# Kernel optimization log

Measured on AMD Instinct MI355X. Metric: run time of the kernel, lower is better.

## Reference

```python
import jax, jax.numpy as jnp
import numpy as np

D_MODEL = 1024
HEADS = 16
D_K = D_MODEL // HEADS
SCALE = 1.0 / np.sqrt(D_K)


def setup_inputs() -> dict:
    key = jax.random.key(0)
    ks = jax.random.split(key, 12)
    B, S = 4, 2048
    std = 1.0 / np.sqrt(D_MODEL)
    inp = {
        "query": jax.random.normal(ks[0], (B, S, D_MODEL), jnp.float32),
        "key": jax.random.normal(ks[1], (B, S, D_MODEL), jnp.float32),
        "value": jax.random.normal(ks[2], (B, S, D_MODEL), jnp.float32),
        # projection weights stored [in, out] (transpose of torch Linear)
        "Wq": jax.random.normal(ks[3], (D_MODEL, D_MODEL), jnp.float32) * std,
        "bq": jax.random.normal(ks[4], (D_MODEL,), jnp.float32) * std,
        "Wk": jax.random.normal(ks[5], (D_MODEL, D_MODEL), jnp.float32) * std,
        "bk": jax.random.normal(ks[6], (D_MODEL,), jnp.float32) * std,
        "Wv": jax.random.normal(ks[7], (D_MODEL, D_MODEL), jnp.float32) * std,
        "bv": jax.random.normal(ks[8], (D_MODEL,), jnp.float32) * std,
        "Wo": jax.random.normal(ks[9], (D_MODEL, D_MODEL), jnp.float32) * std,
        "bo": jax.random.normal(ks[10], (D_MODEL,), jnp.float32) * std,
    }
    return inp


def _proj(x, W, b):
    # [B,S,D] -> [B,S,H,Dk]
    B, S, _ = x.shape
    return (x @ W + b).reshape(B, S, HEADS, D_K)


def reference(query, key, value, Wq, bq, Wk, bk, Wv, bv, Wo, bo):
    B, S, _ = query.shape
    Q = _proj(query, Wq, bq)
    K = _proj(key, Wk, bk)
    V = _proj(value, Wv, bv)
    scores = jnp.einsum('bihd,bjhd->bijh', Q, K) * SCALE
    # FAITHFUL to original: nn.Softmax(dim=1) normalizes over the QUERY axis i
    attn = jax.nn.softmax(scores, axis=1)
    # dropout is identity at inference
    x = jnp.einsum('bijh,bjhd->bihd', attn, V).reshape(B, S, D_MODEL)
    return x @ Wo + bo
```

## Files before the change

kernel.cpp:

```cpp
#include <hip/hip_runtime.h>


#define B_   4
#define S_   2048
#define D_   1024
#define H_   16
#define DK_  64
#define BH_  64
#define SC2_    0.18033688f

typedef __bf16 bf16x2 __attribute__((ext_vector_type(2)));
typedef __bf16 bf16x4 __attribute__((ext_vector_type(4)));
typedef __bf16 bf16x8 __attribute__((ext_vector_type(8)));
typedef float  f32x4  __attribute__((ext_vector_type(4)));
typedef unsigned int u32;

#define MFMA16(a,b,c) __builtin_amdgcn_mfma_f32_16x16x32_bf16((a),(b),(c),0,0,0)

__device__ __forceinline__ bf16x8 ld8(const __bf16* p){ return *(const bf16x8*)p; }

__device__ __forceinline__ void gll16(const __bf16* g, __bf16* l) {
    __builtin_amdgcn_global_load_lds(
        (const __attribute__((address_space(1))) u32*)g,
        (__attribute__((address_space(3))) u32*)l, 16, 0, 0);
}

#define PIPE_BAR(N) do {                                                      \
    asm volatile("s_waitcnt vmcnt(" #N ") lgkmcnt(0)" ::: "memory");          \
    __builtin_amdgcn_s_barrier();                                             \
    __builtin_amdgcn_sched_barrier(0);                                        \
} while (0)

__global__ __launch_bounds__(256) void wtrans3(
    const float* __restrict__ W0, const float* __restrict__ W1,
    const float* __restrict__ W2, __bf16* __restrict__ Wt)
{
    __shared__ __align__(16) __bf16 Ls[64][80];
    const int t = threadIdx.x;
    const int k0 = blockIdx.x * 64, n0 = blockIdx.y * 64, z = blockIdx.z;
    const float* W = (z == 0) ? W0 : ((z == 1) ? W1 : W2);
    __bf16* out = Wt + (size_t)z * D_ * D_;

#pragma unroll
    for (int p = 0; p < 4; ++p) {
        int id = p*256 + t;
        int k = id >> 4, nq = id & 15;
        f32x4 v = *(const f32x4*)&W[(size_t)(k0 + k)*D_ + n0 + nq*4];
#pragma unroll
        for (int u = 0; u < 4; ++u) Ls[nq*4 + u][k] = (__bf16)v[u];
    }
    __syncthreads();
#pragma unroll
    for (int p = 0; p < 2; ++p) {
        int id = p*256 + t;
        int n = id >> 3, c = id & 7;
        *(bf16x8*)&out[(size_t)(n0 + n)*D_ + k0 + c*8] =
            *(const bf16x8*)&Ls[n][c*8];
    }
}

template<int ABF16, int MODE>
__device__ __forceinline__ void gemm_pipe(
    const void* __restrict__ Ap, const __bf16* __restrict__ Wt,
    const float* __restrict__ bias, void* __restrict__ C,
    float scale, int m0, int n0)
{
    __shared__ __align__(16) __bf16 As[3][128*32];
    __shared__ __align__(16) __bf16 Bs[3][128*32];

    const int t = threadIdx.x, lane = t & 63, w = t >> 6;
    const int wm = w >> 1, wn = w & 1;
    const int fr = lane & 15, fq = lane >> 4;

    const __bf16* Ab = (const __bf16*)Ap;
    const float*  Af = (const float*)Ap;

    f32x4 acc[4][4];
#pragma unroll
    for (int i = 0; i < 4; ++i)
#pragma unroll
        for (int j = 0; j < 4; ++j) acc[i][j] = (f32x4){0.f,0.f,0.f,0.f};

#define PSTAGE_B(kk, bsel)                                                    \
    _Pragma("unroll")                                                         \
    for (int p = 0; p < 2; ++p) {                                             \
        int id = p*256 + t;                                                   \
        int n = id >> 2, l = (id & 3) ^ (n & 3);                              \
        gll16(&Wt[(size_t)(n0 + n)*D_ + (kk) + l*8],                          \
              &Bs[bsel][(size_t)(p*256 + (t & ~63))*8]);                      \
    }

#define PSTAGE_A_BF(kk, bsel)                                                 \
    _Pragma("unroll")                                                         \
    for (int p = 0; p < 2; ++p) {                                             \
        int id = p*256 + t;                                                   \
        int row = id >> 2, l = (id & 3) ^ (row & 3);                          \
        gll16(&Ab[(size_t)(m0 + row)*D_ + (kk) + l*8],                        \
              &As[bsel][(size_t)(p*256 + (t & ~63))*8]);                      \
    }

#define PLOAD_A(kk, xa)                                                       \
    _Pragma("unroll")                                                         \
    for (int p = 0; p < 2; ++p) {                                             \
        int id = p*256 + t;                                                   \
        int row = id >> 2, l = (id & 3) ^ (row & 3);                          \
        const float* ap = &Af[(size_t)(m0 + row)*D_ + (kk) + l*8];            \
        xa[2*p]   = *(const f32x4*)ap;                                        \
        xa[2*p+1] = *(const f32x4*)(ap + 4);                                  \
    }

#define PCVT_WR(xa, bsel)                                                     \
    _Pragma("unroll")                                                         \
    for (int p = 0; p < 2; ++p) {                                             \
        f32x4 x0 = xa[2*p], x1 = xa[2*p+1];                                   \
        bf16x8 v = { (__bf16)x0[0], (__bf16)x0[1], (__bf16)x0[2],             \
                     (__bf16)x0[3], (__bf16)x1[0], (__bf16)x1[1],             \
                     (__bf16)x1[2], (__bf16)x1[3] };                          \
        *(bf16x8*)&As[bsel][(size_t)(p*256 + t)*8] = v;                       \
    }

    f32x4 xa0[4], xa1[4];

    if (ABF16) {
        PSTAGE_A_BF(0, 0)  PSTAGE_B(0, 0)
        PSTAGE_A_BF(32, 1) PSTAGE_B(32, 1)
        PIPE_BAR(4);
    } else {
        PSTAGE_B(0, 0)  PLOAD_A(0, xa0)
        PSTAGE_B(32, 1) PLOAD_A(32, xa1)
        PCVT_WR(xa0, 0)
        PIPE_BAR(6);
    }

#pragma unroll
    for (int tt = 0; tt < 32; ++tt) {
        const int cur = tt % 3, nx1 = (tt + 1) % 3, nx2 = (tt + 2) % 3;

        if (ABF16) {
            if (tt < 30) {
                PSTAGE_A_BF(32*(tt + 2), nx2)
                PSTAGE_B(32*(tt + 2), nx2)
            }
        } else {
            if (tt < 30) {
                PSTAGE_B(32*(tt + 2), nx2)
                if (tt & 1) { PLOAD_A(32*(tt + 2), xa1) }
                else        { PLOAD_A(32*(tt + 2), xa0) }
            }
            if (tt < 31) {
                if (tt & 1) { PCVT_WR(xa0, nx1) }
                else        { PCVT_WR(xa1, nx1) }
            }
        }

        {
            bf16x8 af[4], bfr[4];
#pragma unroll
            for (int mt = 0; mt < 4; ++mt) {
                int row = wm*64 + mt*16 + fr;
                af[mt] = ld8(&As[cur][row*32 + 8*(fq ^ (row & 3))]);
            }
#pragma unroll
            for (int nt = 0; nt < 4; ++nt) {
                int n = wn*64 + nt*16 + fr;
                bfr[nt] = ld8(&Bs[cur][n*32 + 8*(fq ^ (n & 3))]);
            }
#pragma unroll
            for (int mt = 0; mt < 4; ++mt)
#pragma unroll
                for (int nt = 0; nt < 4; ++nt)
                    acc[mt][nt] = MFMA16(af[mt], bfr[nt], acc[mt][nt]);
        }

        if (ABF16) { PIPE_BAR(4); } else { PIPE_BAR(6); }
    }
#undef PSTAGE_B
#undef PSTAGE_A_BF
#undef PLOAD_A
#undef PCVT_WR

#pragma unroll
    for (int mt = 0; mt < 4; ++mt)
#pragma unroll
        for (int nt = 0; nt < 4; ++nt) {
            int colg = n0 + wn*64 + nt*16 + fr;
            float bv = bias[colg];
#pragma unroll
            for (int r = 0; r < 4; ++r) {
                int rowg = m0 + wm*64 + mt*16 + fq*4 + r;
                float o = (acc[mt][nt][r] + bv) * scale;
                if (MODE == 0) {
                    ((float*)C)[(size_t)rowg*D_ + colg] = o;
                } else {
                    int b = rowg >> 11, sp = rowg & (S_-1);
                    int h = colg >> 6, dk = colg & 63;
                    ((__bf16*)C)[(((size_t)(b*H_ + h))*S_ + sp)*DK_ + dk] = (__bf16)o;
                }
            }
        }
}

template<int ABF16, int MODE>
__global__ __launch_bounds__(256) void gemm128(
    const void* __restrict__ Ap, const __bf16* __restrict__ Wt,
    const float* __restrict__ bias, void* __restrict__ C, float scale)
{
    const int gid = blockIdx.x;
    gemm_pipe<ABF16, MODE>(Ap, Wt, bias, C, scale,
                           (gid & 63) * 128, ((gid >> 6) & 7) * 128);
}

__global__ __launch_bounds__(256) void gemm_proj3(
    const float* __restrict__ q, const float* __restrict__ k,
    const float* __restrict__ v, const __bf16* __restrict__ Wt3,
    const float* __restrict__ bq, const float* __restrict__ bk,
    const float* __restrict__ bv,
    __bf16* __restrict__ Qb, __bf16* __restrict__ Kb, __bf16* __restrict__ Vb)
{
    const int gid = blockIdx.x;
    const int z = gid >> 9, inner = gid & 511;
    const float*  A    = (z == 0) ? q  : ((z == 1) ? k  : v);
    const __bf16* Wt   = Wt3 + (size_t)z * D_ * D_;
    const float*  bias = (z == 0) ? bq : ((z == 1) ? bk : bv);
    __bf16*       C    = (z == 0) ? Qb : ((z == 1) ? Kb : Vb);
    const float scale  = (z == 0) ? SC2_ : 1.0f;
    gemm_pipe<0, 1>(A, Wt, bias, C, scale,
                    (inner & 63) * 128, (inner >> 6) * 128);
}

__global__ __launch_bounds__(256) void colsum_rcp(
    const __bf16* __restrict__ Q, const __bf16* __restrict__ K,
    float* __restrict__ Lg)
{
    __shared__ __align__(16) __bf16 Qs[2][64*64];
    const int t = threadIdx.x, lane = t & 63, w = t >> 6;
    const int fr = lane & 15, fq = lane >> 4;
    const int gid = blockIdx.x;
    const int bh = gid & 63;
    const int jw = (gid >> 6)*64 + w*16;
    const __bf16* Qb = Q + (size_t)bh*S_*DK_;
    const __bf16* Kb = K + (size_t)bh*S_*DK_;

    bf16x8 kh0, kh1;
    {
        const __bf16* kr = &Kb[(size_t)(jw + fr)*DK_];
        kh0 = ld8(kr + fq*8);
        kh1 = ld8(kr + 32 + fq*8);
    }

    float accl[4] = {};

#pragma unroll
    for (int p = 0; p < 2; ++p) {
        int c = p*256 + t;
        int i = c >> 3, l = (c & 7) ^ (i & 7);
        gll16(&Qb[(size_t)i*DK_ + l*8], &Qs[0][(size_t)(p*256 + (t & ~63))*8]);
    }
    __syncthreads();

    for (int i0 = 0; i0 < S_; i0 += 64) {
        const int cur = (i0 >> 6) & 1;
        if (i0 + 64 < S_) {
#pragma unroll
            for (int p = 0; p < 2; ++p) {
                int c = p*256 + t;
                int i = c >> 3, l = (c & 7) ^ (i & 7);
                gll16(&Qb[(size_t)(i0 + 64 + i)*DK_ + l*8],
                      &Qs[cur ^ 1][(size_t)(p*256 + (t & ~63))*8]);
            }
        }
#pragma unroll
        for (int it = 0; it < 4; ++it) {
            int i = it*16 + fr;
            bf16x8 q0 = ld8(&Qs[cur][i*64 + 8*(fq ^ (i & 7))]);
            bf16x8 q1 = ld8(&Qs[cur][i*64 + 8*((4 + fq) ^ (i & 7))]);
            f32x4 s = MFMA16(kh0, q0, ((f32x4){0.f,0.f,0.f,0.f}));
            s = MFMA16(kh1, q1, s);
#pragma unroll
            for (int r = 0; r < 4; ++r)
                accl[r] += __builtin_amdgcn_exp2f(s[r]);
        }
        __syncthreads();
    }
#pragma unroll
    for (int r = 0; r < 4; ++r) {
        accl[r] += __shfl_xor(accl[r], 1, 64);
        accl[r] += __shfl_xor(accl[r], 2, 64);
        accl[r] += __shfl_xor(accl[r], 4, 64);
        accl[r] += __shfl_xor(accl[r], 8, 64);
    }
    if (fr == 0) {
#pragma unroll
        for (int r = 0; r < 4; ++r)
            Lg[(size_t)bh*S_ + jw + fq*4 + r] = -__log2f(accl[r]);
    }
}

__global__ __launch_bounds__(512, 4) void attn_pv(
    const __bf16* __restrict__ Q, const __bf16* __restrict__ K,
    const __bf16* __restrict__ V, const float* __restrict__ Lg,
    __bf16* __restrict__ X)
{
    __shared__ __align__(16) __bf16 Ks[2][64*64];
    __shared__ __align__(16) __bf16 Vs[2][64*64];
    __shared__ __align__(16) __bf16 Pl[8][32*64];

    const int t = threadIdx.x, lane = t & 63, w = t >> 6;
    const int fr = lane & 15, fq = lane >> 4;
    const int gid = blockIdx.x;
    const int bh = gid & 63;
    const int iw = (gid >> 6)*256 + w*32;
    const __bf16* Qb = Q + (size_t)bh*S_*DK_;
    const __bf16* Kb = K + (size_t)bh*S_*DK_;
    const __bf16* Vb = V + (size_t)bh*S_*DK_;
    const float*  Rb = Lg + (size_t)bh*S_;

    bf16x8 qf[2][2];
#pragma unroll
    for (int it = 0; it < 2; ++it)
#pragma unroll
        for (int kf = 0; kf < 2; ++kf)
            qf[it][kf] = ld8(&Qb[(size_t)(iw + it*16 + fr)*DK_ + kf*32 + fq*8]);

    const int dq = t & 15, jp = t >> 4;
    const int krow = t >> 3;
    const int kchk = (t & 7) ^ (krow & 7);

    f32x4 acc[2][4];
#pragma unroll
    for (int it = 0; it < 2; ++it)
#pragma unroll
        for (int dt = 0; dt < 4; ++dt) acc[it][dt] = (f32x4){0.f,0.f,0.f,0.f};

    gll16(&Kb[(size_t)krow*DK_ + kchk*8], &Ks[0][(t & ~63)*8]);
    __syncthreads();

    for (int jg = 0; jg < S_; jg += 64) {
        const int cur = (jg >> 6) & 1;

        bf16x4 v0 = *(const bf16x4*)&Vb[(size_t)(jg + 2*jp    )*DK_ + dq*4];
        bf16x4 v1 = *(const bf16x4*)&Vb[(size_t)(jg + 2*jp + 1)*DK_ + dq*4];
        f32x4 lg[4];
#pragma unroll
        for (int jt = 0; jt < 4; ++jt)
            lg[jt] = *(const f32x4*)&Rb[jg + jt*16 + fq*4];
        if (jg + 64 < S_)
            gll16(&Kb[(size_t)(jg + 64 + krow)*DK_ + kchk*8],
                  &Ks[cur ^ 1][(t & ~63)*8]);

#pragma unroll
        for (int jt = 0; jt < 4; ++jt) {
            const __bf16* kb = &Ks[cur][(jt*16 + fr)*64];
            bf16x8 af0 = ld8(kb + ((fq    ) ^ (fr & 7))*8);
            bf16x8 af1 = ld8(kb + ((fq + 4) ^ (fr & 7))*8);
#pragma unroll
            for (int it = 0; it < 2; ++it) {
                f32x4 s = MFMA16(af0, qf[it][0], lg[jt]);
                s = MFMA16(af1, qf[it][1], s);
                bf16x4 pv;
#pragma unroll
                for (int r = 0; r < 4; ++r)
                    pv[r] = (__bf16)__builtin_amdgcn_exp2f(s[r]);
                int il = it*16 + fr;
                *(bf16x4*)&Pl[w][il*64 + (((jt*4 + fq) ^ (2*(fr & 7))))*4] = pv;
            }
        }

#pragma unroll
        for (int u = 0; u < 4; ++u) {
            int d = dq*4 + u;
            int f = (d ^ dq) & 7;
            *(bf16x2*)&Vs[cur][d*64 + (((jp >> 2) ^ f))*8 + (jp & 3)*2] =
                (bf16x2){ v0[u], v1[u] };
        }
        __syncthreads();

        __builtin_amdgcn_s_setprio(1);
#pragma unroll
        for (int kh = 0; kh < 2; ++kh) {
            bf16x8 pa0 = ld8(&Pl[w][(     fr)*64 + (((fq + 4*kh) ^ (fr & 7)))*8]);
            bf16x8 pa1 = ld8(&Pl[w][(16 + fr)*64 + (((fq + 4*kh) ^ (fr & 7)))*8]);
#pragma unroll
            for (int dt = 0; dt < 4; ++dt) {
                int d = dt*16 + fr;
                int f = (d ^ (d >> 2)) & 7;
                bf16x8 vb = ld8(&Vs[cur][d*64 + (((kh*4 + fq) ^ f))*8]);
                acc[0][dt] = MFMA16(pa0, vb, acc[0][dt]);
                acc[1][dt] = MFMA16(pa1, vb, acc[1][dt]);
            }
        }
        __builtin_amdgcn_s_setprio(0);
    }

    const int b = bh >> 4, h = bh & 15;
#pragma unroll
    for (int it = 0; it < 2; ++it)
#pragma unroll
        for (int dt = 0; dt < 4; ++dt)
#pragma unroll
            for (int r = 0; r < 4; ++r) {
                int i = iw + it*16 + fq*4 + r;
                X[((size_t)b*S_ + i)*D_ + h*DK_ + dt*16 + fr] =
                    (__bf16)acc[it][dt][r];
            }
}

extern "C" void kernel_launch(void* const* d_in, const int* in_sizes, int n_in,
                              void* d_out, int out_size, void* d_ws, size_t ws_size,
                              hipStream_t stream)
{
    const float* query = (const float*)d_in[0];
    const float* key   = (const float*)d_in[1];
    const float* value = (const float*)d_in[2];
    const float* Wq = (const float*)d_in[3];  const float* bq = (const float*)d_in[4];
    const float* Wk = (const float*)d_in[5];  const float* bk = (const float*)d_in[6];
    const float* Wv = (const float*)d_in[7];  const float* bv = (const float*)d_in[8];
    const float* Wo = (const float*)d_in[9];  const float* bo = (const float*)d_in[10];

    char* ws = (char*)d_ws;
    char* dob = (char*)d_out;
    const size_t MiB = 1024 * 1024;
    __bf16* Qb = (__bf16*)(ws);
    __bf16* Kb = (__bf16*)(ws + 16 * MiB);
    __bf16* Vb = (__bf16*)(ws + 32 * MiB);
    __bf16* Xb = (__bf16*)(ws + 48 * MiB);
    float*  Lgb = (float*)d_out;
    __bf16* Wt3 = (__bf16*)(dob + 1 * MiB);
    __bf16* WtO = (__bf16*)(ws);

    wtrans3<<<dim3(16,16,3), 256, 0, stream>>>(Wq, Wk, Wv, Wt3);

    gemm_proj3<<<1536, 256, 0, stream>>>(query, key, value, Wt3,
                                         bq, bk, bv, Qb, Kb, Vb);

    colsum_rcp<<<2048, 256, 0, stream>>>(Qb, Kb, Lgb);

    attn_pv<<<512, 512, 0, stream>>>(Qb, Kb, Vb, Lgb, Xb);

    wtrans3<<<dim3(16,16,1), 256, 0, stream>>>(Wo, Wo, Wo, WtO);

    gemm128<1,0><<<512, 256, 0, stream>>>(Xb, WtO, bo, d_out, 1.0f);
}
```

Baseline: 385.5 us.

## Replace LDS-staged triple-buffered GEMM with direct global-to-register streaming

The projection and output GEMMs no longer stage A and W tiles through shared memory with a three-stage pipeline and barriers. Each wave now loads its MFMA fragments straight from global memory, converting fp32 A inline, and the loop is unrolled by 4 so the compiler can overlap the loads. This removes the LDS traffic and the block barriers, but it loses reuse across waves: each A and W element is fetched by several waves through cache, and the per-lane 16-byte strided reads are poorly coalesced.

```diff
diff --git a/kernel.cpp b/kernel.cpp
--- a/kernel.cpp
+++ b/kernel.cpp
@@ -25,12 +25,6 @@
         (__attribute__((address_space(3))) u32*)l, 16, 0, 0);
 }
 
-#define PIPE_BAR(N) do {                                                      \
-    asm volatile("s_waitcnt vmcnt(" #N ") lgkmcnt(0)" ::: "memory");          \
-    __builtin_amdgcn_s_barrier();                                             \
-    __builtin_amdgcn_sched_barrier(0);                                        \
-} while (0)
-
 __global__ __launch_bounds__(256) void wtrans3(
     const float* __restrict__ W0, const float* __restrict__ W1,
     const float* __restrict__ W2, __bf16* __restrict__ Wt)
@@ -60,14 +54,11 @@
 }
 
 template<int ABF16, int MODE>
-__device__ __forceinline__ void gemm_pipe(
+__device__ __forceinline__ void gemm_stream(
     const void* __restrict__ Ap, const __bf16* __restrict__ Wt,
     const float* __restrict__ bias, void* __restrict__ C,
     float scale, int m0, int n0)
 {
-    __shared__ __align__(16) __bf16 As[3][128*32];
-    __shared__ __align__(16) __bf16 Bs[3][128*32];
-
     const int t = threadIdx.x, lane = t & 63, w = t >> 6;
     const int wm = w >> 1, wn = w & 1;
     const int fr = lane & 15, fq = lane >> 4;
@@ -75,109 +66,45 @@
     const __bf16* Ab = (const __bf16*)Ap;
     const float*  Af = (const float*)Ap;
 
+    size_t arow[4], brow[4];
+#pragma unroll
+    for (int mt = 0; mt < 4; ++mt)
+        arow[mt] = (size_t)(m0 + wm*64 + mt*16 + fr) * D_ + fq*8;
+#pragma unroll
+    for (int nt = 0; nt < 4; ++nt)
+        brow[nt] = (size_t)(n0 + wn*64 + nt*16 + fr) * D_ + fq*8;
+
     f32x4 acc[4][4];
 #pragma unroll
     for (int i = 0; i < 4; ++i)
 #pragma unroll
         for (int j = 0; j < 4; ++j) acc[i][j] = (f32x4){0.f,0.f,0.f,0.f};
 
-#define PSTAGE_B(kk, bsel)                                                    \
-    _Pragma("unroll")                                                         \
-    for (int p = 0; p < 2; ++p) {                                             \
-        int id = p*256 + t;                                                   \
-        int n = id >> 2, l = (id & 3) ^ (n & 3);                              \
-        gll16(&Wt[(size_t)(n0 + n)*D_ + (kk) + l*8],                          \
-              &Bs[bsel][(size_t)(p*256 + (t & ~63))*8]);                      \
-    }
-
-#define PSTAGE_A_BF(kk, bsel)                                                 \
-    _Pragma("unroll")                                                         \
-    for (int p = 0; p < 2; ++p) {                                             \
-        int id = p*256 + t;                                                   \
-        int row = id >> 2, l = (id & 3) ^ (row & 3);                          \
-        gll16(&Ab[(size_t)(m0 + row)*D_ + (kk) + l*8],                        \
-              &As[bsel][(size_t)(p*256 + (t & ~63))*8]);                      \
-    }
-
-#define PLOAD_A(kk, xa)                                                       \
-    _Pragma("unroll")                                                         \
-    for (int p = 0; p < 2; ++p) {                                             \
-        int id = p*256 + t;                                                   \
-        int row = id >> 2, l = (id & 3) ^ (row & 3);                          \
-        const float* ap = &Af[(size_t)(m0 + row)*D_ + (kk) + l*8];            \
-        xa[2*p]   = *(const f32x4*)ap;                                        \
-        xa[2*p+1] = *(const f32x4*)(ap + 4);                                  \
-    }
-
-#define PCVT_WR(xa, bsel)                                                     \
-    _Pragma("unroll")                                                         \
-    for (int p = 0; p < 2; ++p) {                                             \
-        f32x4 x0 = xa[2*p], x1 = xa[2*p+1];                                   \
-        bf16x8 v = { (__bf16)x0[0], (__bf16)x0[1], (__bf16)x0[2],             \
-                     (__bf16)x0[3], (__bf16)x1[0], (__bf16)x1[1],             \
-                     (__bf16)x1[2], (__bf16)x1[3] };                          \
-        *(bf16x8*)&As[bsel][(size_t)(p*256 + t)*8] = v;                       \
-    }
-
-    f32x4 xa0[4], xa1[4];
-
-    if (ABF16) {
-        PSTAGE_A_BF(0, 0)  PSTAGE_B(0, 0)
-        PSTAGE_A_BF(32, 1) PSTAGE_B(32, 1)
-        PIPE_BAR(4);
-    } else {
-        PSTAGE_B(0, 0)  PLOAD_A(0, xa0)
-        PSTAGE_B(32, 1) PLOAD_A(32, xa1)
-        PCVT_WR(xa0, 0)
-        PIPE_BAR(6);
-    }
-
-#pragma unroll
-    for (int tt = 0; tt < 32; ++tt) {
-        const int cur = tt % 3, nx1 = (tt + 1) % 3, nx2 = (tt + 2) % 3;
-
-        if (ABF16) {
-            if (tt < 30) {
-                PSTAGE_A_BF(32*(tt + 2), nx2)
-                PSTAGE_B(32*(tt + 2), nx2)
-            }
-        } else {
-            if (tt < 30) {
-                PSTAGE_B(32*(tt + 2), nx2)
-                if (tt & 1) { PLOAD_A(32*(tt + 2), xa1) }
-                else        { PLOAD_A(32*(tt + 2), xa0) }
-            }
-            if (tt < 31) {
-                if (tt & 1) { PCVT_WR(xa0, nx1) }
-                else        { PCVT_WR(xa1, nx1) }
-            }
-        }
-
-        {
-            bf16x8 af[4], bfr[4];
-#pragma unroll
-            for (int mt = 0; mt < 4; ++mt) {
-                int row = wm*64 + mt*16 + fr;
-                af[mt] = ld8(&As[cur][row*32 + 8*(fq ^ (row & 3))]);
-            }
-#pragma unroll
-            for (int nt = 0; nt < 4; ++nt) {
-                int n = wn*64 + nt*16 + fr;
-                bfr[nt] = ld8(&Bs[cur][n*32 + 8*(fq ^ (n & 3))]);
-            }
-#pragma unroll
-            for (int mt = 0; mt < 4; ++mt)
-#pragma unroll
-                for (int nt = 0; nt < 4; ++nt)
-                    acc[mt][nt] = MFMA16(af[mt], bfr[nt], acc[mt][nt]);
-        }
-
-        if (ABF16) { PIPE_BAR(4); } else { PIPE_BAR(6); }
-    }
-#undef PSTAGE_B
-#undef PSTAGE_A_BF
-#undef PLOAD_A
-#undef PCVT_WR
+#pragma unroll 4
+    for (int kk = 0; kk < D_; kk += 32) {
+        bf16x8 af[4], bfr[4];
+#pragma unroll
+        for (int mt = 0; mt < 4; ++mt) {
+            if (ABF16) {
+                af[mt] = ld8(&Ab[arow[mt] + kk]);
+            } else {
+                const float* ap = &Af[arow[mt] + kk];
+                f32x4 x0 = *(const f32x4*)ap;
+                f32x4 x1 = *(const f32x4*)(ap + 4);
+                af[mt] = (bf16x8){ (__bf16)x0[0], (__bf16)x0[1], (__bf16)x0[2],
+                                   (__bf16)x0[3], (__bf16)x1[0], (__bf16)x1[1],
+                                   (__bf16)x1[2], (__bf16)x1[3] };
+            }
+        }
+#pragma unroll
+        for (int nt = 0; nt < 4; ++nt)
+            bfr[nt] = ld8(&Wt[brow[nt] + kk]);
+#pragma unroll
+        for (int mt = 0; mt < 4; ++mt)
+#pragma unroll
+            for (int nt = 0; nt < 4; ++nt)
+                acc[mt][nt] = MFMA16(af[mt], bfr[nt], acc[mt][nt]);
+    }
 
 #pragma unroll
     for (int mt = 0; mt < 4; ++mt)
@@ -206,8 +133,8 @@
     const float* __restrict__ bias, void* __restrict__ C, float scale)
 {
     const int gid = blockIdx.x;
-    gemm_pipe<ABF16, MODE>(Ap, Wt, bias, C, scale,
-                           (gid & 63) * 128, ((gid >> 6) & 7) * 128);
+    gemm_stream<ABF16, MODE>(Ap, Wt, bias, C, scale,
+                             (gid & 63) * 128, ((gid >> 6) & 7) * 128);
 }
 
 __global__ __launch_bounds__(256) void gemm_proj3(
@@ -224,8 +151,8 @@
     const float*  bias = (z == 0) ? bq : ((z == 1) ? bk : bv);
     __bf16*       C    = (z == 0) ? Qb : ((z == 1) ? Kb : Vb);
     const float scale  = (z == 0) ? SC2_ : 1.0f;
-    gemm_pipe<0, 1>(A, Wt, bias, C, scale,
-                    (inner & 63) * 128, (inner >> 6) * 128);
+    gemm_stream<0, 1>(A, Wt, bias, C, scale,
+                      (inner & 63) * 128, (inner >> 6) * 128);
 }
 
 __global__ __launch_bounds__(256) void colsum_rcp(
```

Result: slower. 583.4 us (+51.3%).
